# Optimization experiments

Hardware: AMD Instinct MI355X
Metric: run time of the kernel (lower is better)

Reference implementation:

```python
import jax, jax.numpy as jnp
import numpy as np

N_NODES = 100000
N_EDGES = 1600000
N_FEAT = 165
HIDDEN = 128
N_CLASSES = 2
NEG_SLOPE = 0.2


def setup_inputs() -> dict:
    key = jax.random.key(0)
    ks = jax.random.split(key, 16)
    s = 0.05
    return {
        'x': jax.random.normal(ks[0], (N_NODES, N_FEAT), jnp.float32),
        'edge_src': jax.random.randint(ks[1], (N_EDGES,), 0, N_NODES, jnp.int32),
        'edge_dst': jax.random.randint(ks[2], (N_EDGES,), 0, N_NODES, jnp.int32),
        'W1l': jax.random.normal(ks[3], (N_FEAT, HIDDEN), jnp.float32) * s,
        'b1l': jnp.zeros((HIDDEN,), jnp.float32),
        'W1r': jax.random.normal(ks[4], (N_FEAT, HIDDEN), jnp.float32) * s,
        'b1r': jnp.zeros((HIDDEN,), jnp.float32),
        'att1': jax.random.normal(ks[5], (HIDDEN,), jnp.float32) * s,
        'bias1': jnp.zeros((HIDDEN,), jnp.float32),
        'W2l': jax.random.normal(ks[6], (HIDDEN, N_CLASSES), jnp.float32) * s,
        'b2l': jnp.zeros((N_CLASSES,), jnp.float32),
        'W2r': jax.random.normal(ks[7], (HIDDEN, N_CLASSES), jnp.float32) * s,
        'b2r': jnp.zeros((N_CLASSES,), jnp.float32),
        'att2': jax.random.normal(ks[8], (N_CLASSES,), jnp.float32) * s,
        'bias2': jnp.zeros((N_CLASSES,), jnp.float32),
    }


def gatv2_conv(x, src, dst, Wl, bl, Wr, br, att, bias, n_nodes):
    # PyG GATv2Conv, heads=1: x_l for source/message, x_r for target
    xl = x @ Wl + bl            # [N, D_out]
    xr = x @ Wr + br            # [N, D_out]
    e = jax.nn.leaky_relu(xl[src] + xr[dst], NEG_SLOPE)  # [E, D_out]
    score = e @ att             # [E]
    # segment softmax over destination nodes (stable)
    m = jax.ops.segment_max(score, dst, num_segments=n_nodes)
    a = jnp.exp(score - m[dst])
    denom = jax.ops.segment_sum(a, dst, num_segments=n_nodes)
    alpha = a / denom[dst]      # [E]
    out = jax.ops.segment_sum(alpha[:, None] * xl[src], dst, num_segments=n_nodes)
    return out + bias


def reference(x, edge_src, edge_dst, W1l, b1l, W1r, b1r, att1, bias1,
              W2l, b2l, W2r, b2r, att2, bias2):
    n = x.shape[0]
    # GATv2Conv adds self loops by default; every node has >=1 incoming edge
    loops = jnp.arange(n, dtype=edge_src.dtype)
    src = jnp.concatenate([edge_src, loops])
    dst = jnp.concatenate([edge_dst, loops])
    h = gatv2_conv(x, src, dst, W1l, b1l, W1r, b1r, att1, bias1, n)
    h = jax.nn.relu(h)
    # F.dropout with training=False is identity (eval mode)
    out = gatv2_conv(h, src, dst, W2l, b2l, W2r, b2r, att2, bias2, n)
    return out
```

## Files before the change

kernel.cpp:

```cpp
#include <hip/hip_runtime.h>
#include <hip/hip_bf16.h>

#define N_NODES 100000
#define NPAD 100032
#define N_EDGES 1600000
#define ETOT (N_EDGES + N_NODES)
#define NFEAT 165
#define KP 192
#define HID 128
#define NCLS 2
#define NEG 0.2f

#define NBUCK 391
#define CHUNK 16384
#define NCHUNK 104
#define GS_BLOCKS 2048

typedef short bf16x8 __attribute__((ext_vector_type(8)));
typedef float f32x4 __attribute__((ext_vector_type(4)));

#define OFF_FLAG 0
#define OFF_W 16
#define WO_ATT1 42496
#define WO_BIAS1 42624
#define WO_W2L 42752
#define WO_B2L 43008
#define WO_W2R 43010
#define WO_B2R 43266
#define WO_ATT2 43268
#define WO_BIAS2 43270

#define OFF_XB   43392
#define OFF_W2A  OFF_XB
#define OFF_WT   (OFF_XB + NPAD * KP / 2)
#define OFF_BCAT (OFF_WT + 256 * KP / 2)
#define OFF_XLB  (OFF_BCAT + 256)
#define OFF_XRB  (OFF_XLB + NPAD * HID / 2)
#define OFF_PAIRS (OFF_XRB + NPAD * HID / 2)
#define OFF_CSR  (OFF_PAIRS + 2 * ETOT)
#define OFF_ROWPTR (OFF_CSR + ETOT)
#define OFF_S    (OFF_ROWPTR + N_NODES + 8)
#define OFF_XL2  (OFF_S + NBUCK * NCHUNK + 8)
#define OFF_XR2  (OFF_XL2 + N_NODES * NCLS)
#define OFF_H    (OFF_XR2 + N_NODES * NCLS)
#define OFF_DL   (OFF_H + N_NODES * HID)
#define OFF_DR   (OFF_DL + NPAD)

__device__ __forceinline__ float bload16(unsigned short u) {
    return __uint_as_float(((unsigned)u) << 16);
}

__device__ __forceinline__ float lrelu(float v) {
    return fmaf(0.4f, fabsf(v), 0.6f * v);
}

__device__ __forceinline__ void unpack8(uint4 q, float* f) {
    f[0] = __uint_as_float(q.x << 16); f[1] = __uint_as_float(q.x & 0xffff0000u);
    f[2] = __uint_as_float(q.y << 16); f[3] = __uint_as_float(q.y & 0xffff0000u);
    f[4] = __uint_as_float(q.z << 16); f[5] = __uint_as_float(q.z & 0xffff0000u);
    f[6] = __uint_as_float(q.w << 16); f[7] = __uint_as_float(q.w & 0xffff0000u);
}

__device__ __forceinline__ unsigned short f2b(float f) {
    __hip_bfloat16 b = __float2bfloat16(f);
    return *(unsigned short*)&b;
}

__device__ __forceinline__ unsigned pack2(float a, float b) {
    return (unsigned)f2b(a) | ((unsigned)f2b(b) << 16);
}

__device__ __forceinline__ unsigned detect_flag(const unsigned short* x16, int lane) {
    unsigned short hh = x16[lane];
    unsigned e = (hh >> 7) & 0xFF;
    bool pl = ((hh & 0x7FFF) == 0) || (e >= 100 && e <= 140);
    unsigned long long m = __ballot(pl);
    return (__popcll(m) >= 52) ? 1u : 0u;
}

#define PREP_WT 49152
#define PREP_BC (PREP_WT + 256)
#define PREP_TOT (PREP_BC + 776)
#define PREP_BLKS ((PREP_TOT + 255) / 256)
__global__ void __launch_bounds__(256) k_prep_hist(
        const int* __restrict__ edst, int* __restrict__ bh,
        const unsigned short* __restrict__ x16,
        const void* W1l, const void* b1l, const void* W1r, const void* b1r,
        const void* att1, const void* bias1, const void* W2l, const void* b2l,
        const void* W2r, const void* b2r, const void* att2, const void* bias2,
        unsigned* __restrict__ flagp, unsigned short* __restrict__ wt,
        float* __restrict__ bcat, float* __restrict__ wb,
        float* __restrict__ w2a) {
    __shared__ int hist[NBUCK];
    if (blockIdx.x < NCHUNK) {
        for (int i = threadIdx.x; i < NBUCK; i += 256) hist[i] = 0;
        __syncthreads();
        int base = blockIdx.x * CHUNK;
        for (int i = threadIdx.x; i < CHUNK; i += 256) {
            int e = base + i;
            if (e >= ETOT) break;
            int d = (e < N_EDGES) ? edst[e] : (e - N_EDGES);
            atomicAdd(&hist[d >> 8], 1);
        }
        __syncthreads();
        for (int b = threadIdx.x; b < NBUCK; b += 256)
            bh[b * NCHUNK + blockIdx.x] = hist[b];
        return;
    }
    int lane = threadIdx.x & 63;
    unsigned isbf = detect_flag(x16, lane);
    int i = (blockIdx.x - NCHUNK) * 256 + threadIdx.x;
    if (i == 0) *flagp = isbf;
    if (i >= PREP_TOT) return;
    if (i < PREP_WT) {
        int n = i / KP, k = i - n * KP;
        unsigned short v = 0;
        if (k < NFEAT) {
            const void* src = (n < HID) ? W1l : W1r;
            size_t off = (size_t)k * HID + (n & (HID - 1));
            v = isbf ? ((const unsigned short*)src)[off]
                     : f2b(((const float*)src)[off]);
        }
        wt[i] = v;
    } else if (i < PREP_BC) {
        int n = i - PREP_WT;
        const void* src = (n < HID) ? b1l : b1r;
        int off = n & (HID - 1);
        bcat[n] = isbf ? bload16(((const unsigned short*)src)[off])
                       : ((const float*)src)[off];
    } else {
        int j = i - PREP_BC;
        const void* src; int off; int dst;
        if      (j < 128) { src = att1;  off = j;       dst = WO_ATT1 + j; }
        else if (j < 256) { src = bias1; off = j - 128; dst = WO_BIAS1 + (j - 128); }
        else if (j < 512) { src = W2l;   off = j - 256; dst = WO_W2L + (j - 256); }
        else if (j < 514) { src = b2l;   off = j - 512; dst = WO_B2L + (j - 512); }
        else if (j < 770) { src = W2r;   off = j - 514; dst = WO_W2R + (j - 514); }
        else if (j < 772) { src = b2r;   off = j - 770; dst = WO_B2R + (j - 770); }
        else if (j < 774) { src = att2;  off = j - 772; dst = WO_ATT2 + (j - 772); }
        else              { src = bias2; off = j - 774; dst = WO_BIAS2 + (j - 774); }
        float val = isbf ? bload16(((const unsigned short*)src)[off])
                         : ((const float*)src)[off];
        wb[dst] = val;
        if (j >= 256 && j < 512) w2a[j - 256] = val;
        else if (j >= 514 && j < 770) w2a[256 + (j - 514)] = val;
    }
}

__global__ void __launch_bounds__(512) k_pa_scan(int* __restrict__ S,
                                                 int* __restrict__ rowptr) {
    __shared__ int lds[512];
    const int TOT4 = (NBUCK * NCHUNK) / 4;
    int t = threadIdx.x;
    int b4 = t * 20;
    uint4* S4 = (uint4*)S;
    int sum = 0;
    for (int k = 0; k < 20; k++) {
        int i = b4 + k;
        if (i < TOT4) {
            uint4 v = S4[i];
            sum += (int)(v.x + v.y + v.z + v.w);
        }
    }
    lds[t] = sum;
    __syncthreads();
    for (int off = 1; off < 512; off <<= 1) {
        int v = lds[t];
        if (t >= off) v += lds[t - off];
        __syncthreads();
        lds[t] = v;
        __syncthreads();
    }
    int carry = (t == 0) ? 0 : lds[t - 1];
    for (int k = 0; k < 20; k++) {
        int i = b4 + k;
        if (i < TOT4) {
            uint4 v = S4[i];
            uint4 o;
            o.x = carry; carry += v.x;
            o.y = carry; carry += v.y;
            o.z = carry; carry += v.z;
            o.w = carry; carry += v.w;
            S4[i] = o;
        }
    }
    if (t == 0) rowptr[N_NODES] = ETOT;
}

#define XS_STRIDE 200
__global__ void __launch_bounds__(256) k_scatter_gemm1(
        const int* __restrict__ esrc, const int* __restrict__ edst,
        const int* __restrict__ S, unsigned* __restrict__ pairs,
        const void* __restrict__ x, const unsigned* __restrict__ flagp,
        const unsigned short* __restrict__ wt, const float* __restrict__ bcat,
        const float* __restrict__ attp,
        __hip_bfloat16* __restrict__ xlb, __hip_bfloat16* __restrict__ xrb,
        float* __restrict__ dl, float* __restrict__ dr) {
    __shared__ union {
        struct { unsigned short xs[64 * XS_STRIDE]; float dpart[4][64]; } g;
        int cur[NBUCK];
    } u;

    if (blockIdx.x < NCHUNK) {
        for (int i = threadIdx.x; i < NBUCK; i += 256)
            u.cur[i] = S[i * NCHUNK + blockIdx.x];
        __syncthreads();
        int base = blockIdx.x * CHUNK;
        for (int i = threadIdx.x; i < CHUNK; i += 256) {
            int e = base + i;
            if (e >= ETOT) break;
            int s = (e < N_EDGES) ? esrc[e] : (e - N_EDGES);
            int d = (e < N_EDGES) ? edst[e] : (e - N_EDGES);
            int p = atomicAdd(&u.cur[d >> 8], 1);
            pairs[p] = (unsigned)s | ((unsigned)(d & 255) << 24);
        }
        return;
    }

    int tid = threadIdx.x;
    int wave = tid >> 6, lane = tid & 63;
    int quad = lane >> 4, li = lane & 15;
    int node0 = (blockIdx.x - NCHUNK) * 64;
    unsigned isbf = *flagp;
    const float* xf = (const float*)x;
    const unsigned short* x16 = (const unsigned short*)x;

    for (int i = tid; i < 64 * 27; i += 256) {
        int r = i / 27, c = 165 + (i - r * 27);
        u.g.xs[r * XS_STRIDE + c] = 0;
    }
    if (node0 + 64 <= N_NODES) {
        if (isbf) {
            const uint4* src = (const uint4*)(x16 + (size_t)node0 * NFEAT);
            for (int i = tid; i < 1320; i += 256) {
                uint4 v = src[i];
                int f = i * 8;
                unsigned short hh[8] = {
                    (unsigned short)(v.x & 0xffff), (unsigned short)(v.x >> 16),
                    (unsigned short)(v.y & 0xffff), (unsigned short)(v.y >> 16),
                    (unsigned short)(v.z & 0xffff), (unsigned short)(v.z >> 16),
                    (unsigned short)(v.w & 0xffff), (unsigned short)(v.w >> 16)};
#pragma unroll
                for (int t = 0; t < 8; t++) {
                    int ff = f + t, r = ff / NFEAT, c = ff - r * NFEAT;
                    u.g.xs[r * XS_STRIDE + c] = hh[t];
                }
            }
        } else {
            const float4* src = (const float4*)(xf + (size_t)node0 * NFEAT);
            for (int i = tid; i < 2640; i += 256) {
                float4 v = src[i];
                int f = i * 4;
                unsigned short hh[4] = {f2b(v.x), f2b(v.y), f2b(v.z), f2b(v.w)};
#pragma unroll
                for (int t = 0; t < 4; t++) {
                    int ff = f + t, r = ff / NFEAT, c = ff - r * NFEAT;
                    u.g.xs[r * XS_STRIDE + c] = hh[t];
                }
            }
        }
    } else {
        for (int i = tid; i < 64 * NFEAT; i += 256) {
            int r = i / NFEAT, c = i - r * NFEAT;
            int grow = node0 + r;
            unsigned short v = 0;
            if (grow < N_NODES) {
                size_t g = (size_t)grow * NFEAT + c;
                v = isbf ? x16[g] : f2b(xf[g]);
            }
            u.g.xs[r * XS_STRIDE + c] = v;
        }
    }

    bf16x8 wfrag[4][6];
#pragma unroll
    for (int q = 0; q < 4; q++) {
        int n = wave * 64 + q * 16 + li;
#pragma unroll
        for (int kk = 0; kk < 6; kk++)
            wfrag[q][kk] = *(const bf16x8*)&wt[(size_t)n * KP + kk * 32 + quad * 8];
    }
    float4 bv[4], attq4[4];
    int colbase = (wave & 1) * 64;
#pragma unroll
    for (int q = 0; q < 4; q++) {
        bv[q] = *(const float4*)&bcat[wave * 64 + q * 16 + quad * 4];
        attq4[q] = *(const float4*)&attp[colbase + q * 16 + quad * 4];
    }
    __syncthreads();

    for (int mt = 0; mt < 4; mt++) {
        bf16x8 xfrag[6];
#pragma unroll
        for (int kk = 0; kk < 6; kk++)
            xfrag[kk] = *(const bf16x8*)&u.g.xs[(mt * 16 + li) * XS_STRIDE + kk * 32 + quad * 8];
        int node = node0 + mt * 16 + li;
        __hip_bfloat16* dst = (wave < 2) ? xlb : xrb;
        float dp = 0.f;
#pragma unroll
        for (int q = 0; q < 4; q++) {
            f32x4 a = {0.f, 0.f, 0.f, 0.f};
#pragma unroll
            for (int kk = 0; kk < 6; kk++)
                a = __builtin_amdgcn_mfma_f32_16x16x32_bf16(wfrag[q][kk], xfrag[kk], a, 0, 0, 0);
            float f0 = a[0] + bv[q].x, f1 = a[1] + bv[q].y;
            float f2 = a[2] + bv[q].z, f3 = a[3] + bv[q].w;
            dp = fmaf(f0, attq4[q].x, dp);
            dp = fmaf(f1, attq4[q].y, dp);
            dp = fmaf(f2, attq4[q].z, dp);
            dp = fmaf(f3, attq4[q].w, dp);
            uint2 val = { pack2(f0, f1), pack2(f2, f3) };
            int col = colbase + q * 16 + quad * 4;
            *(uint2*)&dst[(size_t)node * HID + col] = val;
        }
        dp += __shfl_xor(dp, 16);
        dp += __shfl_xor(dp, 32);
        if (lane < 16) u.g.dpart[wave][mt * 16 + li] = dp;
    }
    __syncthreads();
    if (tid < 64)
        dl[node0 + tid] = u.g.dpart[0][tid] + u.g.dpart[1][tid];
    else if (tid < 128)
        dr[node0 + tid - 64] = u.g.dpart[2][tid - 64] + u.g.dpart[3][tid - 64];
}

__global__ void __launch_bounds__(256) k_bsort(const int* __restrict__ S,
                                               const unsigned* __restrict__ pairs,
                                               int* __restrict__ rowptr,
                                               int* __restrict__ csr) {
    __shared__ int hist[256];
    __shared__ int cur[256];
    int b = blockIdx.x, t = threadIdx.x;
    int beg = S[b * NCHUNK];
    int end = (b == NBUCK - 1) ? ETOT : S[(b + 1) * NCHUNK];
    hist[t] = 0;
    __syncthreads();
    for (int j = beg + t; j < end; j += 256)
        atomicAdd(&hist[pairs[j] >> 24], 1);
    __syncthreads();
    for (int off = 1; off < 256; off <<= 1) {
        int v = hist[t];
        if (t >= off) v += hist[t - off];
        __syncthreads();
        hist[t] = v;
        __syncthreads();
    }
    int excl = (t == 0) ? 0 : hist[t - 1];
    int node = b * 256 + t;
    if (node < N_NODES) rowptr[node] = beg + excl;
    cur[t] = beg + excl;
    __syncthreads();
    for (int j = beg + t; j < end; j += 256) {
        unsigned pr = pairs[j];
        int p = atomicAdd(&cur[pr >> 24], 1);
        csr[p] = (int)(pr & 0xFFFFFFu);
    }
}

__global__ void __launch_bounds__(256) k_gat1(const int* __restrict__ rowptr,
                                              const int* __restrict__ csr,
                                              const __hip_bfloat16* __restrict__ xlb,
                                              const __hip_bfloat16* __restrict__ xrb,
                                              const float* __restrict__ att,
                                              const float* __restrict__ bias,
                                              const float* __restrict__ dotsl,
                                              const float* __restrict__ dotsr,
                                              unsigned short* __restrict__ h16) {
    int wave = threadIdx.x >> 6, lane = threadIdx.x & 63;
    int sub = lane >> 4, li = lane & 15;
    float atv[8];
    {
        float4 t0 = ((const float4*)att)[li * 2];
        float4 t1 = ((const float4*)att)[li * 2 + 1];
        atv[0] = 0.4f * t0.x; atv[1] = 0.4f * t0.y;
        atv[2] = 0.4f * t0.z; atv[3] = 0.4f * t0.w;
        atv[4] = 0.4f * t1.x; atv[5] = 0.4f * t1.y;
        atv[6] = 0.4f * t1.z; atv[7] = 0.4f * t1.w;
    }

    for (int d = blockIdx.x * 4 + wave; d < N_NODES; d += GS_BLOCKS * 4) {
        uint4 qr = ((const uint4*)(xrb + (size_t)d * HID))[li];
        float xrv[8]; unpack8(qr, xrv);
        float drd = dotsr[d];
        int beg = rowptr[d], end = rowptr[d + 1];
        int iters = (end - beg + 3) >> 2;
        float l = 0.f, o[8];
#pragma unroll
        for (int t = 0; t < 8; t++) o[t] = 0.f;

        int j = beg + sub;
        bool valid = j < end;
        int s = valid ? csr[j] : 0;
        uint4 q = *(const uint4*)(xlb + (size_t)s * HID + li * 8);
        float dlc = dotsl[s];

        for (int it = 0; it < iters; it++) {
            float c[8]; unpack8(q, c);
            bool v = valid;
            float dle = dlc;
            j += 4;
            valid = j < end;
            int sn = valid ? csr[j] : 0;
            q = *(const uint4*)(xlb + (size_t)sn * HID + li * 8);
            dlc = dotsl[sn];

            float pa = 0.f;
#pragma unroll
            for (int t = 0; t < 8; t++) {
                float vv = c[t] + xrv[t];
                pa = fmaf(atv[t], fabsf(vv), pa);
            }
            pa += __shfl_xor(pa, 1);
            pa += __shfl_xor(pa, 2);
            pa += __shfl_xor(pa, 4);
            pa += __shfl_xor(pa, 8);
            float p = fmaf(0.6f, dle + drd, pa);
            float a = v ? __expf(p) : 0.f;
            l += a;
#pragma unroll
            for (int t = 0; t < 8; t++) o[t] = fmaf(a, c[t], o[t]);
        }
        l += __shfl_xor(l, 16);
        l += __shfl_xor(l, 32);
#pragma unroll
        for (int t = 0; t < 8; t++) {
            o[t] += __shfl_xor(o[t], 16);
            o[t] += __shfl_xor(o[t], 32);
        }
        if (sub == 0) {
            float inv = 1.f / l;
            float4 bv0 = ((const float4*)bias)[li * 2];
            float4 bv1 = ((const float4*)bias)[li * 2 + 1];
            float r0 = fmaxf(fmaf(o[0], inv, bv0.x), 0.f);
            float r1 = fmaxf(fmaf(o[1], inv, bv0.y), 0.f);
            float r2 = fmaxf(fmaf(o[2], inv, bv0.z), 0.f);
            float r3 = fmaxf(fmaf(o[3], inv, bv0.w), 0.f);
            float r4 = fmaxf(fmaf(o[4], inv, bv1.x), 0.f);
            float r5 = fmaxf(fmaf(o[5], inv, bv1.y), 0.f);
            float r6 = fmaxf(fmaf(o[6], inv, bv1.z), 0.f);
            float r7 = fmaxf(fmaf(o[7], inv, bv1.w), 0.f);
            uint4 val = { pack2(r0, r1), pack2(r2, r3),
                          pack2(r4, r5), pack2(r6, r7) };
            *(uint4*)&h16[(size_t)d * HID + li * 8] = val;
        }
    }
}

__global__ void __launch_bounds__(256) k_gemm2(const unsigned short* __restrict__ h16,
                                               const float* __restrict__ wb,
                                               const float* __restrict__ w2a,
                                               float* __restrict__ xl2, float* __restrict__ xr2) {
    int wave = threadIdx.x >> 6, lane = threadIdx.x & 63;
    int node = blockIdx.x * 4 + wave;
    if (node >= N_NODES) return;
    unsigned hw = ((const unsigned*)(h16 + (size_t)node * HID))[lane];
    float h0 = __uint_as_float(hw << 16);
    float h1 = __uint_as_float(hw & 0xffff0000u);
    float4 wl = ((const float4*)w2a)[lane];
    float4 wr = ((const float4*)(w2a + 256))[lane];
    float al0 = h0 * wl.x + h1 * wl.z;
    float al1 = h0 * wl.y + h1 * wl.w;
    float ar0 = h0 * wr.x + h1 * wr.z;
    float ar1 = h0 * wr.y + h1 * wr.w;
#pragma unroll
    for (int off = 32; off > 0; off >>= 1) {
        al0 += __shfl_down(al0, off);
        al1 += __shfl_down(al1, off);
        ar0 += __shfl_down(ar0, off);
        ar1 += __shfl_down(ar1, off);
    }
    if (lane == 0) {
        xl2[node * 2 + 0] = al0 + wb[WO_B2L + 0];
        xl2[node * 2 + 1] = al1 + wb[WO_B2L + 1];
        xr2[node * 2 + 0] = ar0 + wb[WO_B2R + 0];
        xr2[node * 2 + 1] = ar1 + wb[WO_B2R + 1];
    }
}

__global__ void __launch_bounds__(256) k_gat2(const int* __restrict__ rowptr,
                                              const int* __restrict__ csr,
                                              const float* __restrict__ xl2,
                                              const float* __restrict__ xr2,
                                              const float* __restrict__ wb,
                                              const unsigned* __restrict__ flag,
                                              void* __restrict__ dout) {
    int t = blockIdx.x * 256 + threadIdx.x;
    int d = t >> 2, part = t & 3;
    if (d >= N_NODES) return;
    float xr0 = xr2[d * 2 + 0], xr1 = xr2[d * 2 + 1];
    float at0 = wb[WO_ATT2], at1 = wb[WO_ATT2 + 1];
    int beg = rowptr[d], end = rowptr[d + 1];
    float l = 0.f, o0 = 0.f, o1 = 0.f;
    for (int j = beg + part; j < end; j += 4) {
        int s = csr[j];
        float b0 = xl2[s * 2 + 0], b1 = xl2[s * 2 + 1];
        float p = at0 * lrelu(b0 + xr0) + at1 * lrelu(b1 + xr1);
        float a = __expf(p);
        l += a;
        o0 = fmaf(a, b0, o0);
        o1 = fmaf(a, b1, o1);
    }
    l += __shfl_xor(l, 1);  o0 += __shfl_xor(o0, 1);  o1 += __shfl_xor(o1, 1);
    l += __shfl_xor(l, 2);  o0 += __shfl_xor(o0, 2);  o1 += __shfl_xor(o1, 2);
    if (part == 0) {
        float inv = 1.f / l;
        float v0 = fmaf(o0, inv, wb[WO_BIAS2 + 0]);
        float v1 = fmaf(o1, inv, wb[WO_BIAS2 + 1]);
        if (*flag) {
            ((__hip_bfloat16*)dout)[d * 2 + 0] = __float2bfloat16(v0);
            ((__hip_bfloat16*)dout)[d * 2 + 1] = __float2bfloat16(v1);
        } else {
            ((float*)dout)[d * 2 + 0] = v0;
            ((float*)dout)[d * 2 + 1] = v1;
        }
    }
}

extern "C" void kernel_launch(void* const* d_in, const int* in_sizes, int n_in,
                              void* d_out, int out_size, void* d_ws, size_t ws_size,
                              hipStream_t stream) {
    char* w = (char*)d_ws;
    unsigned* flag = (unsigned*)(w + (size_t)OFF_FLAG * 4);
    float* wb = (float*)(w + (size_t)OFF_W * 4);
    float* w2a = (float*)(w + (size_t)OFF_W2A * 4);
    unsigned short* wt = (unsigned short*)(w + (size_t)OFF_WT * 4);
    float* bcat = (float*)(w + (size_t)OFF_BCAT * 4);
    __hip_bfloat16* xlb = (__hip_bfloat16*)(w + (size_t)OFF_XLB * 4);
    __hip_bfloat16* xrb = (__hip_bfloat16*)(w + (size_t)OFF_XRB * 4);
    unsigned* pairs = (unsigned*)(w + (size_t)OFF_PAIRS * 4);
    int* csr = (int*)(w + (size_t)OFF_CSR * 4);
    int* rowptr = (int*)(w + (size_t)OFF_ROWPTR * 4);
    int* S = (int*)(w + (size_t)OFF_S * 4);
    float* xl2 = (float*)(w + (size_t)OFF_XL2 * 4);
    float* xr2 = (float*)(w + (size_t)OFF_XR2 * 4);
    unsigned short* h16 = (unsigned short*)(w + (size_t)OFF_H * 4);
    float* dl = (float*)(w + (size_t)OFF_DL * 4);
    float* dr = (float*)(w + (size_t)OFF_DR * 4);
    const int* esrc = (const int*)d_in[1];
    const int* edst = (const int*)d_in[2];

    k_prep_hist<<<NCHUNK + PREP_BLKS, 256, 0, stream>>>(
        edst, S, (const unsigned short*)d_in[0],
        d_in[3], d_in[4], d_in[5], d_in[6], d_in[7], d_in[8],
        d_in[9], d_in[10], d_in[11], d_in[12], d_in[13], d_in[14],
        flag, wt, bcat, wb, w2a);

    k_pa_scan<<<1, 512, 0, stream>>>(S, rowptr);

    k_scatter_gemm1<<<NCHUNK + NPAD / 64, 256, 0, stream>>>(
        esrc, edst, S, pairs, d_in[0], flag, wt, bcat,
        wb + WO_ATT1, xlb, xrb, dl, dr);

    k_bsort<<<NBUCK, 256, 0, stream>>>(S, pairs, rowptr, csr);

    k_gat1<<<GS_BLOCKS, 256, 0, stream>>>(rowptr, csr, xlb, xrb,
                                          wb + WO_ATT1, wb + WO_BIAS1,
                                          dl, dr, h16);

    k_gemm2<<<(N_NODES + 3) / 4, 256, 0, stream>>>(h16, wb, w2a, xl2, xr2);

    k_gat2<<<(4 * N_NODES + 255) / 256, 256, 0, stream>>>(rowptr, csr, xl2, xr2,
                                                          wb, flag, d_out);
}
```

Measured before the change: 362.2 us.

## Build CSR with global per-node atomic counting instead of bucketed two-pass sort

Replaces the chunked bucket histogram, bucket scatter and per-bucket local sort with a direct CSR build. Per-node in-degree is counted with global atomics, a two-level scan produces rowptr and inserts self-loops, and edges are scattered straight into csr via atomic cursors. This removes the intermediate pairs buffer and the k_bsort pass. In exchange it adds a memset and an extra scan launch and relies on heavily contended global atomics, and edge order within each row becomes nondeterministic.

```diff
diff --git a/kernel.cpp b/kernel.cpp
--- a/kernel.cpp
+++ b/kernel.cpp
@@ -11,10 +11,10 @@
 #define NCLS 2
 #define NEG 0.2f
 
-#define NBUCK 391
-#define CHUNK 16384
-#define NCHUNK 104
 #define GS_BLOCKS 2048
+#define NCB 208
+#define SCB 208
+#define NGRP 196
 
 typedef short bf16x8 __attribute__((ext_vector_type(8)));
 typedef float f32x4 __attribute__((ext_vector_type(4)));
@@ -37,10 +37,13 @@
 #define OFF_XLB  (OFF_BCAT + 256)
 #define OFF_XRB  (OFF_XLB + NPAD * HID / 2)
 #define OFF_PAIRS (OFF_XRB + NPAD * HID / 2)
+#define OFF_CNT  OFF_PAIRS
+#define OFF_CUR  (OFF_CNT + N_NODES)
+#define OFF_BS   (OFF_CUR + N_NODES)
 #define OFF_CSR  (OFF_PAIRS + 2 * ETOT)
 #define OFF_ROWPTR (OFF_CSR + ETOT)
 #define OFF_S    (OFF_ROWPTR + N_NODES + 8)
-#define OFF_XL2  (OFF_S + NBUCK * NCHUNK + 8)
+#define OFF_XL2  (OFF_S + 391 * 104 + 8)
 #define OFF_XR2  (OFF_XL2 + N_NODES * NCLS)
 #define OFF_H    (OFF_XR2 + N_NODES * NCLS)
 #define OFF_DL   (OFF_H + N_NODES * HID)
@@ -78,12 +81,13 @@
     return (__popcll(m) >= 52) ? 1u : 0u;
 }
 
+
 #define PREP_WT 49152
 #define PREP_BC (PREP_WT + 256)
 #define PREP_TOT (PREP_BC + 776)
 #define PREP_BLKS ((PREP_TOT + 255) / 256)
-__global__ void __launch_bounds__(256) k_prep_hist(
-        const int* __restrict__ edst, int* __restrict__ bh,
+__global__ void __launch_bounds__(256) k_prep_count(
+        const int* __restrict__ edst, int* __restrict__ cnt,
         const unsigned short* __restrict__ x16,
         const void* W1l, const void* b1l, const void* W1r, const void* b1r,
         const void* att1, const void* bias1, const void* W2l, const void* b2l,
@@ -91,25 +95,15 @@
         unsigned* __restrict__ flagp, unsigned short* __restrict__ wt,
         float* __restrict__ bcat, float* __restrict__ wb,
         float* __restrict__ w2a) {
-    __shared__ int hist[NBUCK];
-    if (blockIdx.x < NCHUNK) {
-        for (int i = threadIdx.x; i < NBUCK; i += 256) hist[i] = 0;
-        __syncthreads();
-        int base = blockIdx.x * CHUNK;
-        for (int i = threadIdx.x; i < CHUNK; i += 256) {
-            int e = base + i;
-            if (e >= ETOT) break;
-            int d = (e < N_EDGES) ? edst[e] : (e - N_EDGES);
-            atomicAdd(&hist[d >> 8], 1);
-        }
-        __syncthreads();
-        for (int b = threadIdx.x; b < NBUCK; b += 256)
-            bh[b * NCHUNK + blockIdx.x] = hist[b];
+    if (blockIdx.x < NCB) {
+        int stride = NCB * 256;
+        for (int e = blockIdx.x * 256 + threadIdx.x; e < N_EDGES; e += stride)
+            atomicAdd(&cnt[edst[e]], 1);
         return;
     }
     int lane = threadIdx.x & 63;
     unsigned isbf = detect_flag(x16, lane);
-    int i = (blockIdx.x - NCHUNK) * 256 + threadIdx.x;
+    int i = (blockIdx.x - NCB) * 256 + threadIdx.x;
     if (i == 0) *flagp = isbf;
     if (i >= PREP_TOT) return;
     if (i < PREP_WT) {
@@ -147,72 +141,75 @@
     }
 }
 
-__global__ void __launch_bounds__(512) k_pa_scan(int* __restrict__ S,
-                                                 int* __restrict__ rowptr) {
-    __shared__ int lds[512];
-    const int TOT4 = (NBUCK * NCHUNK) / 4;
+__global__ void __launch_bounds__(512) k_scan1(const int* __restrict__ cnt,
+                                               int* __restrict__ bs) {
+    __shared__ int ws[8];
     int t = threadIdx.x;
-    int b4 = t * 20;
-    uint4* S4 = (uint4*)S;
-    int sum = 0;
-    for (int k = 0; k < 20; k++) {
-        int i = b4 + k;
-        if (i < TOT4) {
-            uint4 v = S4[i];
-            sum += (int)(v.x + v.y + v.z + v.w);
-        }
-    }
-    lds[t] = sum;
+    int n = blockIdx.x * 512 + t;
+    int v = (n < N_NODES) ? cnt[n] : 0;
+    v += __shfl_down(v, 32);
+    v += __shfl_down(v, 16);
+    v += __shfl_down(v, 8);
+    v += __shfl_down(v, 4);
+    v += __shfl_down(v, 2);
+    v += __shfl_down(v, 1);
+    if ((t & 63) == 0) ws[t >> 6] = v;
+    __syncthreads();
+    if (t == 0) {
+        int s = 0;
+#pragma unroll
+        for (int i = 0; i < 8; i++) s += ws[i];
+        bs[blockIdx.x] = s;
+    }
+}
+
+__global__ void __launch_bounds__(512) k_scanw(const int* __restrict__ cnt,
+                                               const int* __restrict__ bs,
+                                               int* __restrict__ rowptr,
+                                               int* __restrict__ cur,
+                                               int* __restrict__ csr) {
+    __shared__ int sb[512];
+    __shared__ int loc[512];
+    int t = threadIdx.x, b = blockIdx.x;
+    int n = b * 512 + t;
+    sb[t] = (t < NGRP) ? bs[t] : 0;
+    loc[t] = (n < N_NODES) ? cnt[n] : 0;
     __syncthreads();
     for (int off = 1; off < 512; off <<= 1) {
-        int v = lds[t];
-        if (t >= off) v += lds[t - off];
+        int v1 = sb[t], v2 = loc[t];
+        if (t >= off) { v1 += sb[t - off]; v2 += loc[t - off]; }
         __syncthreads();
-        lds[t] = v;
+        sb[t] = v1; loc[t] = v2;
         __syncthreads();
     }
-    int carry = (t == 0) ? 0 : lds[t - 1];
-    for (int k = 0; k < 20; k++) {
-        int i = b4 + k;
-        if (i < TOT4) {
-            uint4 v = S4[i];
-            uint4 o;
-            o.x = carry; carry += v.x;
-            o.y = carry; carry += v.y;
-            o.z = carry; carry += v.z;
-            o.w = carry; carry += v.w;
-            S4[i] = o;
-        }
-    }
-    if (t == 0) rowptr[N_NODES] = ETOT;
+    int base = (b == 0) ? 0 : sb[b - 1];
+    int excl = (t == 0) ? 0 : loc[t - 1];
+    if (n < N_NODES) {
+        int rp = base + excl + n;
+        rowptr[n] = rp;
+        cur[n] = rp + 1;
+        csr[rp] = n;
+    }
+    if (b == 0 && t == 0) rowptr[N_NODES] = ETOT;
 }
 
 #define XS_STRIDE 200
 __global__ void __launch_bounds__(256) k_scatter_gemm1(
         const int* __restrict__ esrc, const int* __restrict__ edst,
-        const int* __restrict__ S, unsigned* __restrict__ pairs,
+        int* __restrict__ cur, int* __restrict__ csr,
         const void* __restrict__ x, const unsigned* __restrict__ flagp,
         const unsigned short* __restrict__ wt, const float* __restrict__ bcat,
         const float* __restrict__ attp,
         __hip_bfloat16* __restrict__ xlb, __hip_bfloat16* __restrict__ xrb,
         float* __restrict__ dl, float* __restrict__ dr) {
-    __shared__ union {
-        struct { unsigned short xs[64 * XS_STRIDE]; float dpart[4][64]; } g;
-        int cur[NBUCK];
-    } u;
-
-    if (blockIdx.x < NCHUNK) {
-        for (int i = threadIdx.x; i < NBUCK; i += 256)
-            u.cur[i] = S[i * NCHUNK + blockIdx.x];
-        __syncthreads();
-        int base = blockIdx.x * CHUNK;
-        for (int i = threadIdx.x; i < CHUNK; i += 256) {
-            int e = base + i;
-            if (e >= ETOT) break;
-            int s = (e < N_EDGES) ? esrc[e] : (e - N_EDGES);
-            int d = (e < N_EDGES) ? edst[e] : (e - N_EDGES);
-            int p = atomicAdd(&u.cur[d >> 8], 1);
-            pairs[p] = (unsigned)s | ((unsigned)(d & 255) << 24);
+    __shared__ struct { unsigned short xs[64 * XS_STRIDE]; float dpart[4][64]; } u;
+
+    if (blockIdx.x < SCB) {
+        int stride = SCB * 256;
+        for (int e = blockIdx.x * 256 + threadIdx.x; e < N_EDGES; e += stride) {
+            int s = esrc[e], d = edst[e];
+            int p = atomicAdd(&cur[d], 1);
+            csr[p] = s;
         }
         return;
     }
@@ -220,14 +217,14 @@
     int tid = threadIdx.x;
     int wave = tid >> 6, lane = tid & 63;
     int quad = lane >> 4, li = lane & 15;
-    int node0 = (blockIdx.x - NCHUNK) * 64;
+    int node0 = (blockIdx.x - SCB) * 64;
     unsigned isbf = *flagp;
     const float* xf = (const float*)x;
     const unsigned short* x16 = (const unsigned short*)x;
 
     for (int i = tid; i < 64 * 27; i += 256) {
         int r = i / 27, c = 165 + (i - r * 27);
-        u.g.xs[r * XS_STRIDE + c] = 0;
+        u.xs[r * XS_STRIDE + c] = 0;
     }
     if (node0 + 64 <= N_NODES) {
         if (isbf) {
@@ -243,7 +240,7 @@
 #pragma unroll
                 for (int t = 0; t < 8; t++) {
                     int ff = f + t, r = ff / NFEAT, c = ff - r * NFEAT;
-                    u.g.xs[r * XS_STRIDE + c] = hh[t];
+                    u.xs[r * XS_STRIDE + c] = hh[t];
                 }
             }
         } else {
@@ -255,7 +252,7 @@
 #pragma unroll
                 for (int t = 0; t < 4; t++) {
                     int ff = f + t, r = ff / NFEAT, c = ff - r * NFEAT;
-                    u.g.xs[r * XS_STRIDE + c] = hh[t];
+                    u.xs[r * XS_STRIDE + c] = hh[t];
                 }
             }
         }
@@ -268,7 +265,7 @@
                 size_t g = (size_t)grow * NFEAT + c;
                 v = isbf ? x16[g] : f2b(xf[g]);
             }
-            u.g.xs[r * XS_STRIDE + c] = v;
+            u.xs[r * XS_STRIDE + c] = v;
         }
     }
 
@@ -293,7 +290,7 @@
         bf16x8 xfrag[6];
 #pragma unroll
         for (int kk = 0; kk < 6; kk++)
-            xfrag[kk] = *(const bf16x8*)&u.g.xs[(mt * 16 + li) * XS_STRIDE + kk * 32 + quad * 8];
+            xfrag[kk] = *(const bf16x8*)&u.xs[(mt * 16 + li) * XS_STRIDE + kk * 32 + quad * 8];
         int node = node0 + mt * 16 + li;
         __hip_bfloat16* dst = (wave < 2) ? xlb : xrb;
         float dp = 0.f;
@@ -315,46 +312,13 @@
         }
         dp += __shfl_xor(dp, 16);
         dp += __shfl_xor(dp, 32);
-        if (lane < 16) u.g.dpart[wave][mt * 16 + li] = dp;
+        if (lane < 16) u.dpart[wave][mt * 16 + li] = dp;
     }
     __syncthreads();
     if (tid < 64)
-        dl[node0 + tid] = u.g.dpart[0][tid] + u.g.dpart[1][tid];
+        dl[node0 + tid] = u.dpart[0][tid] + u.dpart[1][tid];
     else if (tid < 128)
-        dr[node0 + tid - 64] = u.g.dpart[2][tid - 64] + u.g.dpart[3][tid - 64];
-}
-
-__global__ void __launch_bounds__(256) k_bsort(const int* __restrict__ S,
-                                               const unsigned* __restrict__ pairs,
-                                               int* __restrict__ rowptr,
-                                               int* __restrict__ csr) {
-    __shared__ int hist[256];
-    __shared__ int cur[256];
-    int b = blockIdx.x, t = threadIdx.x;
-    int beg = S[b * NCHUNK];
-    int end = (b == NBUCK - 1) ? ETOT : S[(b + 1) * NCHUNK];
-    hist[t] = 0;
-    __syncthreads();
-    for (int j = beg + t; j < end; j += 256)
-        atomicAdd(&hist[pairs[j] >> 24], 1);
-    __syncthreads();
-    for (int off = 1; off < 256; off <<= 1) {
-        int v = hist[t];
-        if (t >= off) v += hist[t - off];
-        __syncthreads();
-        hist[t] = v;
-        __syncthreads();
-    }
-    int excl = (t == 0) ? 0 : hist[t - 1];
-    int node = b * 256 + t;
-    if (node < N_NODES) rowptr[node] = beg + excl;
-    cur[t] = beg + excl;
-    __syncthreads();
-    for (int j = beg + t; j < end; j += 256) {
-        unsigned pr = pairs[j];
-        int p = atomicAdd(&cur[pr >> 24], 1);
-        csr[p] = (int)(pr & 0xFFFFFFu);
-    }
+        dr[node0 + tid - 64] = u.dpart[2][tid - 64] + u.dpart[3][tid - 64];
 }
 
 __global__ void __launch_bounds__(256) k_gat1(const int* __restrict__ rowptr,
@@ -527,10 +491,11 @@
     float* bcat = (float*)(w + (size_t)OFF_BCAT * 4);
     __hip_bfloat16* xlb = (__hip_bfloat16*)(w + (size_t)OFF_XLB * 4);
     __hip_bfloat16* xrb = (__hip_bfloat16*)(w + (size_t)OFF_XRB * 4);
-    unsigned* pairs = (unsigned*)(w + (size_t)OFF_PAIRS * 4);
+    int* cnt = (int*)(w + (size_t)OFF_CNT * 4);
+    int* cur = (int*)(w + (size_t)OFF_CUR * 4);
+    int* bs = (int*)(w + (size_t)OFF_BS * 4);
     int* csr = (int*)(w + (size_t)OFF_CSR * 4);
     int* rowptr = (int*)(w + (size_t)OFF_ROWPTR * 4);
-    int* S = (int*)(w + (size_t)OFF_S * 4);
     float* xl2 = (float*)(w + (size_t)OFF_XL2 * 4);
     float* xr2 = (float*)(w + (size_t)OFF_XR2 * 4);
     unsigned short* h16 = (unsigned short*)(w + (size_t)OFF_H * 4);
@@ -539,19 +504,20 @@
     const int* esrc = (const int*)d_in[1];
     const int* edst = (const int*)d_in[2];
 
-    k_prep_hist<<<NCHUNK + PREP_BLKS, 256, 0, stream>>>(
-        edst, S, (const unsigned short*)d_in[0],
+    hipMemsetAsync(cnt, 0, N_NODES * sizeof(int), stream);
+
+    k_prep_count<<<NCB + PREP_BLKS, 256, 0, stream>>>(
+        edst, cnt, (const unsigned short*)d_in[0],
         d_in[3], d_in[4], d_in[5], d_in[6], d_in[7], d_in[8],
         d_in[9], d_in[10], d_in[11], d_in[12], d_in[13], d_in[14],
         flag, wt, bcat, wb, w2a);
 
-    k_pa_scan<<<1, 512, 0, stream>>>(S, rowptr);
-
-    k_scatter_gemm1<<<NCHUNK + NPAD / 64, 256, 0, stream>>>(
-        esrc, edst, S, pairs, d_in[0], flag, wt, bcat,
+    k_scan1<<<NGRP, 512, 0, stream>>>(cnt, bs);
+    k_scanw<<<NGRP, 512, 0, stream>>>(cnt, bs, rowptr, cur, csr);
+
+    k_scatter_gemm1<<<SCB + NPAD / 64, 256, 0, stream>>>(
+        esrc, edst, cur, csr, d_in[0], flag, wt, bcat,
         wb + WO_ATT1, xlb, xrb, dl, dr);
-
-    k_bsort<<<NBUCK, 256, 0, stream>>>(S, pairs, rowptr, csr);
 
     k_gat1<<<GS_BLOCKS, 256, 0, stream>>>(rowptr, csr, xlb, xrb,
                                           wb + WO_ATT1, wb + WO_BIAS1,
```

Result: slower. 418.0 us (+15.4%).
